# Performance work log

Hardware: AMD Instinct MI355X
Metric: run time of the kernel (lower is better)

Reference implementation:

```python
import jax, jax.numpy as jnp
import numpy as np

D = 1024      # input_dim == attention_dim == num_heads*head_dim
H = 16        # num_heads
HD = 64       # head_dim
FF = 4096     # ff_dim
EPS = 1e-5


def _layernorm(x, gamma, beta):
    mu = jnp.mean(x, axis=-1, keepdims=True)
    var = jnp.var(x, axis=-1, keepdims=True)
    return (x - mu) * jax.lax.rsqrt(var + EPS) * gamma + beta


def setup_inputs() -> dict:
    key = jax.random.key(0)
    ks = jax.random.split(key, 11)
    s_in = 1.0 / np.sqrt(D)
    s_ff = 1.0 / np.sqrt(FF)
    return {
        "x": jax.random.normal(ks[0], (2, 2048, D), dtype=jnp.float32),
        "w_qkv": jax.random.uniform(ks[1], (D, 3 * D), jnp.float32, -s_in, s_in),
        "b_qkv": jax.random.uniform(ks[2], (3 * D,), jnp.float32, -s_in, s_in),
        "w_o": jax.random.uniform(ks[3], (D, D), jnp.float32, -s_in, s_in),
        "b_o": jax.random.uniform(ks[4], (D,), jnp.float32, -s_in, s_in),
        "g1": jnp.ones((D,), jnp.float32),
        "be1": jnp.zeros((D,), jnp.float32),
        "w1": jax.random.uniform(ks[5], (D, FF), jnp.float32, -s_in, s_in),
        "b1": jax.random.uniform(ks[6], (FF,), jnp.float32, -s_in, s_in),
        "w2": jax.random.uniform(ks[7], (FF, D), jnp.float32, -s_ff, s_ff),
        "b2": jax.random.uniform(ks[8], (D,), jnp.float32, -s_ff, s_ff),
        "g2": jnp.ones((D,), jnp.float32),
        "be2": jnp.zeros((D,), jnp.float32),
    }


def reference(x, w_qkv, b_qkv, w_o, b_o, g1, be1, w1, b1, w2, b2, g2, be2):
    N, L, _ = x.shape
    qkv = x @ w_qkv + b_qkv                       # [N, L, 3D]
    q = qkv[..., :D].reshape(N, L, H, HD)
    k = qkv[..., D:2 * D].reshape(N, L, H, HD)
    v = qkv[..., 2 * D:].reshape(N, L, H, HD)
    scores = jnp.einsum('nqhd,nkhd->nhqk', q, k) / np.sqrt(HD)
    attn = jax.nn.softmax(scores, axis=-1)        # [N, H, L, L]
    out = jnp.einsum('nhql,nlhd->nqhd', attn, v).reshape(N, L, D)
    attn_out = out @ w_o + b_o
    # dropout is identity in eval mode
    h = _layernorm(attn_out + x, g1, be1)
    ff = jax.nn.relu(h @ w1 + b1) @ w2 + b2
    return _layernorm(h + ff, g2, be2)
```

## Files before the change

### kernel.cpp

```cpp
#include <hip/hip_runtime.h>
#include <cstddef>
#include <cstdint>

static constexpr int Dm   = 1024;
static constexpr int Hh   = 16;
static constexpr int HDd  = 64;
static constexpr int FFd  = 4096;
static constexpr int Ls   = 2048;
static constexpr int Nb   = 2;
static constexpr int Mrows = Nb * Ls;

typedef short bf16x8 __attribute__((ext_vector_type(8)));
typedef float f32x4  __attribute__((ext_vector_type(4)));

__device__ __forceinline__ ushort f2b(float f) {
    uint32_t u = __builtin_bit_cast(uint32_t, f);
    u = (u + 0x7FFFu + ((u >> 16) & 1u)) >> 16;
    return (ushort)u;
}
__device__ __forceinline__ ushort f2bf(float f) {
    return (ushort)((__builtin_bit_cast(uint32_t, f) + 0x8000u) >> 16);
}
__device__ __forceinline__ float b2f(ushort b) {
    return __builtin_bit_cast(float, (uint32_t)b << 16);
}

__device__ __forceinline__ void gl2lds16(const ushort* g, ushort* l) {
    __builtin_amdgcn_global_load_lds(
        (const __attribute__((address_space(1))) void*)g,
        (__attribute__((address_space(3))) void*)l, 16, 0, 0);
}

__global__ __launch_bounds__(256) void convert_bf16(
    const float* __restrict__ src, ushort* __restrict__ dst, int n)
{
    int i = (blockIdx.x * 256 + threadIdx.x) * 4;
    if (i >= n) return;
    float4 v = *(const float4*)(src + i);
    uint2 o;
    o.x = (uint32_t)f2b(v.x) | ((uint32_t)f2b(v.y) << 16);
    o.y = (uint32_t)f2b(v.z) | ((uint32_t)f2b(v.w) << 16);
    *(uint2*)(dst + i) = o;
}

__global__ __launch_bounds__(256) void transpose_bf16(
    const float* __restrict__ src, ushort* __restrict__ dst, int K, int N)
{
    __shared__ float t[32][33];
    const int k0 = blockIdx.y * 32, n0 = blockIdx.x * 32;
    const int tx = threadIdx.x & 31, ty = threadIdx.x >> 5;
    #pragma unroll
    for (int i = 0; i < 4; ++i)
        t[ty + i * 8][tx] = src[(size_t)(k0 + ty + i * 8) * N + n0 + tx];
    __syncthreads();
    #pragma unroll
    for (int i = 0; i < 4; ++i)
        dst[(size_t)(n0 + ty + i * 8) * K + k0 + tx] = f2b(t[tx][ty + i * 8]);
}

template <int TN, int RELU, int VOUT, int SPLITK>
__global__ __launch_bounds__(256) void gemm_mfma(
    const ushort* __restrict__ A, const ushort* __restrict__ Bt,
    const float* __restrict__ bias,
    ushort* __restrict__ Cb, ushort* __restrict__ vT, int M, int N, int K)
{
    constexpr int NT  = TN / 32;
    constexpr int BSZ = TN * 32;
    __shared__ __align__(16) ushort As[2 * 128 * 32];
    __shared__ __align__(16) ushort Bs[2 * BSZ];

    const int tid  = threadIdx.x;
    int bx, by;
    {
        const int gx = gridDim.x;
        const int nwg = gx * gridDim.y;
        const int lin = blockIdx.y * gx + blockIdx.x;
        const int swz = (lin & 7) * (nwg >> 3) + (lin >> 3);
        by = swz / gx; bx = swz - by * gx;
    }
    const int bm   = by * 128, bn = bx * TN;
    const int wave = tid >> 6, lane = tid & 63;
    const int wm = (wave & 1) * 64;
    const int wn = (wave >> 1) * (TN / 2);
    const int lr = lane & 15, lq = lane >> 4;

    const int KS   = K / SPLITK;
    const int Koff = (SPLITK > 1) ? blockIdx.z * KS : 0;

    const int rr = wave * 16 + (lane >> 2);
    const int sg = lane & 3;
    const ushort* Ag = A  + (size_t)(bm + rr) * K + Koff + sg * 8;
    const ushort* Bg = Bt + (size_t)(bn + rr) * K + Koff + sg * 8;

    f32x4 acc[4][NT];
    #pragma unroll
    for (int i = 0; i < 4; ++i)
        #pragma unroll
        for (int j = 0; j < NT; ++j)
            acc[i][j] = (f32x4){0.f, 0.f, 0.f, 0.f};

    gl2lds16(Ag,                  As + wave * 512);
    gl2lds16(Ag + (size_t)64 * K, As + 2048 + wave * 512);
    gl2lds16(Bg,                  Bs + wave * 512);
    if (TN == 128)
        gl2lds16(Bg + (size_t)64 * K, Bs + 2048 + wave * 512);

    int ib = 0;
    for (int k0 = 0; k0 < KS; k0 += 32, ib ^= 1) {
        __syncthreads();
        if (k0 + 32 < KS) {
            const int nb = ib ^ 1;
            gl2lds16(Ag + k0 + 32,                  As + nb * 4096 + wave * 512);
            gl2lds16(Ag + k0 + 32 + (size_t)64 * K, As + nb * 4096 + 2048 + wave * 512);
            gl2lds16(Bg + k0 + 32,                  Bs + nb * BSZ + wave * 512);
            if (TN == 128)
                gl2lds16(Bg + k0 + 32 + (size_t)64 * K, Bs + nb * BSZ + 2048 + wave * 512);
        }

        const ushort* Ar = As + ib * 4096;
        const ushort* Br = Bs + ib * BSZ;
        bf16x8 af[4], bf[NT];
        #pragma unroll
        for (int mt = 0; mt < 4; ++mt)
            af[mt] = *(const bf16x8*)(Ar + (wm + mt * 16 + lr) * 32 + lq * 8);
        #pragma unroll
        for (int nt = 0; nt < NT; ++nt)
            bf[nt] = *(const bf16x8*)(Br + (wn + nt * 16 + lr) * 32 + lq * 8);

        #pragma unroll
        for (int mt = 0; mt < 4; ++mt)
            #pragma unroll
            for (int nt = 0; nt < NT; ++nt)
                acc[mt][nt] = __builtin_amdgcn_mfma_f32_16x16x32_bf16(
                    af[mt], bf[nt], acc[mt][nt], 0, 0, 0);
    }

    if (SPLITK > 1) {
        ushort* Cp = Cb + (size_t)blockIdx.z * M * N;
        #pragma unroll
        for (int nt = 0; nt < NT; ++nt) {
            const int n = bn + wn + nt * 16 + lr;
            #pragma unroll
            for (int mt = 0; mt < 4; ++mt) {
                const int m0 = bm + wm + mt * 16 + lq * 4;
                #pragma unroll
                for (int r = 0; r < 4; ++r)
                    Cp[(size_t)(m0 + r) * N + n] = f2bf(acc[mt][nt][r]);
            }
        }
        return;
    }
    if (VOUT && bn >= 2 * Dm) {
        #pragma unroll
        for (int nt = 0; nt < NT; ++nt) {
            const int n = bn + wn + nt * 16 + lr;
            const float bv = bias[n];
            const int col = n - 2 * Dm;
            const int h = col >> 6, d = col & 63;
            #pragma unroll
            for (int mt = 0; mt < 4; ++mt) {
                const int m0 = bm + wm + mt * 16 + lq * 4;
                const int batch = m0 >> 11, key0 = m0 & (Ls - 1);
                ushort4 ob;
                ushort* op = (ushort*)&ob;
                #pragma unroll
                for (int r = 0; r < 4; ++r) op[r] = f2bf(acc[mt][nt][r] + bv);
                *(ushort4*)(vT + (((size_t)(batch * Hh + h)) * HDd + d) * Ls + key0) = ob;
            }
        }
        return;
    }
    #pragma unroll
    for (int nt = 0; nt < NT; ++nt) {
        const int n = bn + wn + nt * 16 + lr;
        const float bv = bias[n];
        #pragma unroll
        for (int mt = 0; mt < 4; ++mt) {
            const int m0 = bm + wm + mt * 16 + lq * 4;
            #pragma unroll
            for (int r = 0; r < 4; ++r) {
                float v = acc[mt][nt][r] + bv;
                if (RELU) v = fmaxf(v, 0.0f);
                Cb[(size_t)(m0 + r) * N + n] = f2bf(v);
            }
        }
    }
}

__global__ __launch_bounds__(256) void attn_mfma(
    const ushort* __restrict__ qkv, const ushort* __restrict__ vT,
    ushort* __restrict__ out)
{
    const int tid = threadIdx.x, wave = tid >> 6, lane = tid & 63;
    const int lr = lane & 15, lq = lane >> 4;
    int bx, h, n;
    {
        const int lin = (blockIdx.z * 16 + blockIdx.y) * 16 + blockIdx.x;
        const int swz = (lin & 7) * 64 + (lin >> 3);
        bx = swz & 15; h = (swz >> 4) & 15; n = swz >> 8;
    }
    const int q0 = bx * 128 + wave * 32;
    const size_t RS = 3 * Dm;
    const ushort* base  = qkv + (size_t)n * Ls * RS;
    const ushort* vbase = vT + (size_t)(n * Hh + h) * HDd * Ls;

    __shared__ __align__(16) ushort Kb[64 * 72];
    __shared__ __align__(16) ushort Vt[64 * 72];
    __shared__ __align__(16) ushort Pq[4][32 * 72];

    bf16x8 qf[2][2];
    {
        const float c = 0.18033688011112042f;
        #pragma unroll
        for (int qh = 0; qh < 2; ++qh) {
            const ushort* qg = base + (size_t)(q0 + qh * 16 + lr) * RS + h * HDd + lq * 8;
            bf16x8 t0 = *(const bf16x8*)(qg);
            bf16x8 t1 = *(const bf16x8*)(qg + 32);
            #pragma unroll
            for (int j = 0; j < 8; ++j) {
                qf[0][qh][j] = (short)f2b(b2f((ushort)t0[j]) * c);
                qf[1][qh][j] = (short)f2b(b2f((ushort)t1[j]) * c);
            }
        }
    }

    bf16x8 onesf;
    #pragma unroll
    for (int j = 0; j < 8; ++j) onesf[j] = (short)0x3F80;
    const f32x4 z4 = (f32x4){0.f, 0.f, 0.f, 0.f};

    f32x4 o[4][2];
    #pragma unroll
    for (int dt = 0; dt < 4; ++dt)
        #pragma unroll
        for (int qh = 0; qh < 2; ++qh)
            o[dt][qh] = (f32x4){0.f, 0.f, 0.f, 0.f};
    f32x4 dacc[2];
    dacc[0] = (f32x4){0.f, 0.f, 0.f, 0.f};
    dacc[1] = (f32x4){0.f, 0.f, 0.f, 0.f};

    const int srow = tid >> 2, ssg = tid & 3;
    const ushort* kg = base + (size_t)srow * RS + Dm + h * HDd;
    const ushort* vg = vbase + (size_t)srow * Ls;
    ushort* Pw = Pq[wave];

    int4 ka = *(const int4*)(kg + ssg * 8);
    int4 kb = *(const int4*)(kg + (ssg + 4) * 8);
    int4 va = *(const int4*)(vg + ssg * 8);
    int4 vb = *(const int4*)(vg + (ssg + 4) * 8);

    for (int kt = 0; kt < Ls; kt += 64) {
        __syncthreads();
        *(int4*)(Kb + srow * 72 + ssg * 8)       = ka;
        *(int4*)(Kb + srow * 72 + (ssg + 4) * 8) = kb;
        *(int4*)(Vt + srow * 72 + ssg * 8)       = va;
        *(int4*)(Vt + srow * 72 + (ssg + 4) * 8) = vb;
        __syncthreads();

        if (kt + 64 < Ls) {
            const ushort* kp = kg + (size_t)(kt + 64) * RS;
            const ushort* vp = vg + (kt + 64);
            ka = *(const int4*)(kp + ssg * 8);
            kb = *(const int4*)(kp + (ssg + 4) * 8);
            va = *(const int4*)(vp + ssg * 8);
            vb = *(const int4*)(vp + (ssg + 4) * 8);
        }

        f32x4 s[4][2];
        #pragma unroll
        for (int ks = 0; ks < 2; ++ks)
            #pragma unroll
            for (int mt = 0; mt < 4; ++mt) {
                bf16x8 kf = *(const bf16x8*)(Kb + (mt * 16 + lr) * 72 + ks * 32 + lq * 8);
                #pragma unroll
                for (int qh = 0; qh < 2; ++qh)
                    s[mt][qh] = __builtin_amdgcn_mfma_f32_16x16x32_bf16(
                        kf, qf[ks][qh], ks == 0 ? z4 : s[mt][qh], 0, 0, 0);
            }

        uint2 pb[4][2];
        #pragma unroll
        for (int mt = 0; mt < 4; ++mt)
            #pragma unroll
            for (int qh = 0; qh < 2; ++qh) {
                float p0 = exp2f(s[mt][qh][0]);
                float p1 = exp2f(s[mt][qh][1]);
                float p2 = exp2f(s[mt][qh][2]);
                float p3 = exp2f(s[mt][qh][3]);
                uint32_t w0, w1;
                asm("v_cvt_pk_bf16_f32 %0, %1, %2" : "=v"(w0) : "v"(p0), "v"(p1));
                asm("v_cvt_pk_bf16_f32 %0, %1, %2" : "=v"(w1) : "v"(p2), "v"(p3));
                pb[mt][qh].x = w0;
                pb[mt][qh].y = w1;
            }

        #pragma unroll
        for (int qh = 0; qh < 2; ++qh)
            #pragma unroll
            for (int mt = 0; mt < 4; ++mt)
                *(uint2*)(Pw + (qh * 16 + lr) * 72 + mt * 16 + lq * 4) = pb[mt][qh];

        #pragma unroll
        for (int ks = 0; ks < 2; ++ks) {
            bf16x8 pf[2];
            #pragma unroll
            for (int qh = 0; qh < 2; ++qh)
                pf[qh] = *(const bf16x8*)(Pw + (qh * 16 + lr) * 72 + ks * 32 + lq * 8);
            #pragma unroll
            for (int dt = 0; dt < 4; ++dt) {
                bf16x8 vf = *(const bf16x8*)(Vt + (dt * 16 + lr) * 72 + ks * 32 + lq * 8);
                #pragma unroll
                for (int qh = 0; qh < 2; ++qh)
                    o[dt][qh] = __builtin_amdgcn_mfma_f32_16x16x32_bf16(
                        vf, pf[qh], o[dt][qh], 0, 0, 0);
            }
            #pragma unroll
            for (int qh = 0; qh < 2; ++qh)
                dacc[qh] = __builtin_amdgcn_mfma_f32_16x16x32_bf16(
                    onesf, pf[qh], dacc[qh], 0, 0, 0);
        }
    }

    #pragma unroll
    for (int qh = 0; qh < 2; ++qh) {
        const float inv = 1.0f / dacc[qh][0];
        ushort* orow = out + (size_t)(n * Ls + q0 + qh * 16 + lr) * Dm + h * HDd;
        #pragma unroll
        for (int dt = 0; dt < 4; ++dt) {
            ushort4 ob;
            ushort* op = (ushort*)&ob;
            #pragma unroll
            for (int r = 0; r < 4; ++r) op[r] = f2bf(o[dt][qh][r] * inv);
            *(ushort4*)(orow + dt * 16 + lq * 4) = ob;
        }
    }
}

template <int OTHER_BF16, int OUT_F32>
__global__ __launch_bounds__(256) void add3_ln(
    const ushort* __restrict__ part, const void* __restrict__ other,
    const float* __restrict__ bias,
    const float* __restrict__ gamma, const float* __restrict__ beta,
    float* __restrict__ outf, ushort* __restrict__ outb)
{
    const int row = blockIdx.x;
    const int tid = threadIdx.x;

    ushort4 u0 = ((const ushort4*)(part + (size_t)row * Dm))[tid];
    ushort4 u1 = ((const ushort4*)(part + (size_t)Mrows * Dm + (size_t)row * Dm))[tid];
    float4  bv = ((const float4*)bias)[tid];

    float vo[4];
    if (OTHER_BF16) {
        ushort4 u = ((const ushort4*)((const ushort*)other + (size_t)row * Dm))[tid];
        vo[0] = b2f(u.x); vo[1] = b2f(u.y); vo[2] = b2f(u.z); vo[3] = b2f(u.w);
    } else {
        float4 f = ((const float4*)((const float*)other + (size_t)row * Dm))[tid];
        vo[0] = f.x; vo[1] = f.y; vo[2] = f.z; vo[3] = f.w;
    }
    float v[4];
    v[0] = b2f(u0.x) + b2f(u1.x) + bv.x + vo[0];
    v[1] = b2f(u0.y) + b2f(u1.y) + bv.y + vo[1];
    v[2] = b2f(u0.z) + b2f(u1.z) + bv.z + vo[2];
    v[3] = b2f(u0.w) + b2f(u1.w) + bv.w + vo[3];

    float s  = v[0] + v[1] + v[2] + v[3];
    float sq = v[0]*v[0] + v[1]*v[1] + v[2]*v[2] + v[3]*v[3];

    __shared__ float red[8];
    #pragma unroll
    for (int off = 32; off > 0; off >>= 1) {
        s  += __shfl_down(s, off);
        sq += __shfl_down(sq, off);
    }
    const int wv = tid >> 6;
    if ((tid & 63) == 0) { red[wv] = s; red[4 + wv] = sq; }
    __syncthreads();
    s  = red[0] + red[1] + red[2] + red[3];
    sq = red[4] + red[5] + red[6] + red[7];

    const float mu  = s * (1.0f / Dm);
    const float var = sq * (1.0f / Dm) - mu * mu;
    const float inv = rsqrtf(var + 1e-5f);

    const float4 g  = ((const float4*)gamma)[tid];
    const float4 be = ((const float4*)beta)[tid];
    float ov[4];
    ov[0] = (v[0] - mu) * inv * g.x + be.x;
    ov[1] = (v[1] - mu) * inv * g.y + be.y;
    ov[2] = (v[2] - mu) * inv * g.z + be.z;
    ov[3] = (v[3] - mu) * inv * g.w + be.w;
    if (OUT_F32) {
        float4 o4 = {ov[0], ov[1], ov[2], ov[3]};
        ((float4*)(outf + (size_t)row * Dm))[tid] = o4;
    } else {
        uint2 ob;
        ob.x = (uint32_t)f2bf(ov[0]) | ((uint32_t)f2bf(ov[1]) << 16);
        ob.y = (uint32_t)f2bf(ov[2]) | ((uint32_t)f2bf(ov[3]) << 16);
        *(uint2*)(outb + (size_t)row * Dm + tid * 4) = ob;
    }
}

extern "C" void kernel_launch(void* const* d_in, const int* in_sizes, int n_in,
                              void* d_out, int out_size, void* d_ws, size_t ws_size,
                              hipStream_t stream)
{
    const float* x     = (const float*)d_in[0];
    const float* w_qkv = (const float*)d_in[1];
    const float* b_qkv = (const float*)d_in[2];
    const float* w_o   = (const float*)d_in[3];
    const float* b_o   = (const float*)d_in[4];
    const float* g1    = (const float*)d_in[5];
    const float* be1   = (const float*)d_in[6];
    const float* w1    = (const float*)d_in[7];
    const float* b1    = (const float*)d_in[8];
    const float* w2    = (const float*)d_in[9];
    const float* b2    = (const float*)d_in[10];
    const float* g2    = (const float*)d_in[11];
    const float* be2   = (const float*)d_in[12];
    float* out = (float*)d_out;

    char* p = (char*)d_ws;
    ushort* qkvb  = (ushort*)p;  p += (size_t)Mrows * 3 * Dm * 2;
    ushort* attnb = (ushort*)p;  p += (size_t)Mrows * Dm * 2;
    ushort* part  = (ushort*)p;  p += (size_t)2 * Mrows * Dm * 2;
    ushort* hb    = (ushort*)p;  p += (size_t)Mrows * Dm * 2;
    ushort* ffb   = (ushort*)p;  p += (size_t)Mrows * FFd * 2;
    ushort* xb    = (ushort*)p;  p += (size_t)Mrows * Dm * 2;
    ushort* wqkvT = (ushort*)p;  p += (size_t)(3 * Dm) * Dm * 2;
    ushort* woT   = (ushort*)p;  p += (size_t)Dm * Dm * 2;
    ushort* w1T   = (ushort*)p;  p += (size_t)FFd * Dm * 2;
    ushort* w2T   = (ushort*)p;  p += (size_t)Dm * FFd * 2;
    ushort* vTg   = (ushort*)p;  p += (size_t)Mrows * Dm * 2;

    convert_bf16<<<dim3(Mrows * Dm / 1024), dim3(256), 0, stream>>>(x, xb, Mrows * Dm);
    transpose_bf16<<<dim3(3 * Dm / 32, Dm / 32), dim3(256), 0, stream>>>(w_qkv, wqkvT, Dm, 3 * Dm);
    transpose_bf16<<<dim3(Dm / 32, Dm / 32),     dim3(256), 0, stream>>>(w_o, woT, Dm, Dm);
    transpose_bf16<<<dim3(FFd / 32, Dm / 32),    dim3(256), 0, stream>>>(w1, w1T, Dm, FFd);
    transpose_bf16<<<dim3(Dm / 32, FFd / 32),    dim3(256), 0, stream>>>(w2, w2T, FFd, Dm);

    gemm_mfma<128, 0, 1, 1><<<dim3(3 * Dm / 128, Mrows / 128), dim3(256), 0, stream>>>(
        xb, wqkvT, b_qkv, qkvb, vTg, Mrows, 3 * Dm, Dm);

    attn_mfma<<<dim3(Ls / 128, Hh, Nb), dim3(256), 0, stream>>>(qkvb, vTg, attnb);

    gemm_mfma<64, 0, 0, 2><<<dim3(Dm / 64, Mrows / 128, 2), dim3(256), 0, stream>>>(
        attnb, woT, nullptr, part, nullptr, Mrows, Dm, Dm);

    add3_ln<0, 0><<<dim3(Mrows), dim3(256), 0, stream>>>(
        part, x, b_o, g1, be1, nullptr, hb);

    gemm_mfma<128, 1, 0, 1><<<dim3(FFd / 128, Mrows / 128), dim3(256), 0, stream>>>(
        hb, w1T, b1, ffb, nullptr, Mrows, FFd, Dm);

    gemm_mfma<64, 0, 0, 2><<<dim3(Dm / 64, Mrows / 128, 2), dim3(256), 0, stream>>>(
        ffb, w2T, nullptr, part, nullptr, Mrows, Dm, FFd);

    add3_ln<1, 1><<<dim3(Mrows), dim3(256), 0, stream>>>(
        part, hb, b2, g2, be2, out, nullptr);
}
```

Before: 386.0 us.

## Split attention over two KV halves and add a combine kernel

The attention kernel now splits the key/value sequence into two halves, doubling the grid from 512 to 1024 blocks so more workgroups fill the GPU. Each half writes unnormalized fp32 partial outputs and softmax denominators into reused workspace buffers, and a new combine kernel sums them, normalizes, and writes bf16. This is valid because the kernel uses no running max; it exponentiates raw pre-scaled scores. The exp2 call is also switched to the hardware builtin when available. The cost is an extra launch and a roughly 32MB fp32 partial buffer that must be written and read back.

```diff
diff --git a/kernel.cpp b/kernel.cpp
--- a/kernel.cpp
+++ b/kernel.cpp
@@ -12,6 +12,12 @@
 
 typedef short bf16x8 __attribute__((ext_vector_type(8)));
 typedef float f32x4  __attribute__((ext_vector_type(4)));
+
+#if __has_builtin(__builtin_amdgcn_exp2f)
+#define EXP2(x) __builtin_amdgcn_exp2f(x)
+#else
+#define EXP2(x) exp2f(x)
+#endif
 
 __device__ __forceinline__ ushort f2b(float f) {
     uint32_t u = __builtin_bit_cast(uint32_t, f);
@@ -189,16 +195,18 @@
 
 __global__ __launch_bounds__(256) void attn_mfma(
     const ushort* __restrict__ qkv, const ushort* __restrict__ vT,
-    ushort* __restrict__ out)
+    float* __restrict__ npart, float* __restrict__ dpart)
 {
     const int tid = threadIdx.x, wave = tid >> 6, lane = tid & 63;
     const int lr = lane & 15, lq = lane >> 4;
-    int bx, h, n;
+    int bx, h, z;
     {
         const int lin = (blockIdx.z * 16 + blockIdx.y) * 16 + blockIdx.x;
-        const int swz = (lin & 7) * 64 + (lin >> 3);
-        bx = swz & 15; h = (swz >> 4) & 15; n = swz >> 8;
-    }
+        const int swz = (lin & 7) * 128 + (lin >> 3);
+        bx = swz & 15; h = (swz >> 4) & 15; z = swz >> 8;
+    }
+    const int n = z >> 1, kv = z & 1;
+    const int kt0 = kv * (Ls / 2);
     const int q0 = bx * 128 + wave * 32;
     const size_t RS = 3 * Dm;
     const ushort* base  = qkv + (size_t)n * Ls * RS;
@@ -244,12 +252,16 @@
     const ushort* vg = vbase + (size_t)srow * Ls;
     ushort* Pw = Pq[wave];
 
-    int4 ka = *(const int4*)(kg + ssg * 8);
-    int4 kb = *(const int4*)(kg + (ssg + 4) * 8);
-    int4 va = *(const int4*)(vg + ssg * 8);
-    int4 vb = *(const int4*)(vg + (ssg + 4) * 8);
-
-    for (int kt = 0; kt < Ls; kt += 64) {
+    {
+        const ushort* kp = kg + (size_t)kt0 * RS;
+        const ushort* vp = vg + kt0;
+    }
+    int4 ka = *(const int4*)(kg + (size_t)kt0 * RS + ssg * 8);
+    int4 kb = *(const int4*)(kg + (size_t)kt0 * RS + (ssg + 4) * 8);
+    int4 va = *(const int4*)(vg + kt0 + ssg * 8);
+    int4 vb = *(const int4*)(vg + kt0 + (ssg + 4) * 8);
+
+    for (int kt = kt0; kt < kt0 + Ls / 2; kt += 64) {
         __syncthreads();
         *(int4*)(Kb + srow * 72 + ssg * 8)       = ka;
         *(int4*)(Kb + srow * 72 + (ssg + 4) * 8) = kb;
@@ -257,7 +269,7 @@
         *(int4*)(Vt + srow * 72 + (ssg + 4) * 8) = vb;
         __syncthreads();
 
-        if (kt + 64 < Ls) {
+        if (kt + 64 < kt0 + Ls / 2) {
             const ushort* kp = kg + (size_t)(kt + 64) * RS;
             const ushort* vp = vg + (kt + 64);
             ka = *(const int4*)(kp + ssg * 8);
@@ -283,10 +295,10 @@
         for (int mt = 0; mt < 4; ++mt)
             #pragma unroll
             for (int qh = 0; qh < 2; ++qh) {
-                float p0 = exp2f(s[mt][qh][0]);
-                float p1 = exp2f(s[mt][qh][1]);
-                float p2 = exp2f(s[mt][qh][2]);
-                float p3 = exp2f(s[mt][qh][3]);
+                float p0 = EXP2(s[mt][qh][0]);
+                float p1 = EXP2(s[mt][qh][1]);
+                float p2 = EXP2(s[mt][qh][2]);
+                float p3 = EXP2(s[mt][qh][3]);
                 uint32_t w0, w1;
                 asm("v_cvt_pk_bf16_f32 %0, %1, %2" : "=v"(w0) : "v"(p0), "v"(p1));
                 asm("v_cvt_pk_bf16_f32 %0, %1, %2" : "=v"(w1) : "v"(p2), "v"(p3));
@@ -321,19 +333,43 @@
         }
     }
 
+    const int idx = kv * Nb + n;
     #pragma unroll
     for (int qh = 0; qh < 2; ++qh) {
-        const float inv = 1.0f / dacc[qh][0];
-        ushort* orow = out + (size_t)(n * Ls + q0 + qh * 16 + lr) * Dm + h * HDd;
+        float* nrow = npart + ((size_t)idx * Ls + q0 + qh * 16 + lr) * Dm + h * HDd;
         #pragma unroll
         for (int dt = 0; dt < 4; ++dt) {
-            ushort4 ob;
-            ushort* op = (ushort*)&ob;
-            #pragma unroll
-            for (int r = 0; r < 4; ++r) op[r] = f2bf(o[dt][qh][r] * inv);
-            *(ushort4*)(orow + dt * 16 + lq * 4) = ob;
-        }
-    }
+            float4 o4 = {o[dt][qh][0], o[dt][qh][1], o[dt][qh][2], o[dt][qh][3]};
+            *(float4*)(nrow + dt * 16 + lq * 4) = o4;
+        }
+        if (lane < 16)
+            dpart[((size_t)idx * Hh + h) * Ls + q0 + qh * 16 + lane] = dacc[qh][0];
+    }
+}
+
+__global__ __launch_bounds__(256) void attn_combine(
+    const float* __restrict__ npart, const float* __restrict__ dpart,
+    ushort* __restrict__ out)
+{
+    const int row = blockIdx.x;
+    const int tid = threadIdx.x;
+    const int n = row >> 11, q = row & (Ls - 1);
+    const int h = tid >> 4;
+
+    const size_t b0 = ((size_t)(0 * Nb + n) * Ls + q) * Dm;
+    const size_t b1 = ((size_t)(1 * Nb + n) * Ls + q) * Dm;
+    float4 a = ((const float4*)(npart + b0))[tid];
+    float4 b = ((const float4*)(npart + b1))[tid];
+    const float d0 = dpart[((size_t)(0 * Nb + n) * Hh + h) * Ls + q];
+    const float d1 = dpart[((size_t)(1 * Nb + n) * Hh + h) * Ls + q];
+    const float inv = 1.0f / (d0 + d1);
+
+    ushort4 ob;
+    ob.x = f2bf((a.x + b.x) * inv);
+    ob.y = f2bf((a.y + b.y) * inv);
+    ob.z = f2bf((a.z + b.z) * inv);
+    ob.w = f2bf((a.w + b.w) * inv);
+    *(ushort4*)(out + (size_t)row * Dm + tid * 4) = ob;
 }
 
 template <int OTHER_BF16, int OUT_F32>
@@ -433,6 +469,9 @@
     ushort* w2T   = (ushort*)p;  p += (size_t)Dm * FFd * 2;
     ushort* vTg   = (ushort*)p;  p += (size_t)Mrows * Dm * 2;
 
+    float* npart = (float*)ffb;
+    float* dpart = (float*)part;
+
     convert_bf16<<<dim3(Mrows * Dm / 1024), dim3(256), 0, stream>>>(x, xb, Mrows * Dm);
     transpose_bf16<<<dim3(3 * Dm / 32, Dm / 32), dim3(256), 0, stream>>>(w_qkv, wqkvT, Dm, 3 * Dm);
     transpose_bf16<<<dim3(Dm / 32, Dm / 32),     dim3(256), 0, stream>>>(w_o, woT, Dm, Dm);
@@ -442,7 +481,8 @@
     gemm_mfma<128, 0, 1, 1><<<dim3(3 * Dm / 128, Mrows / 128), dim3(256), 0, stream>>>(
         xb, wqkvT, b_qkv, qkvb, vTg, Mrows, 3 * Dm, Dm);
 
-    attn_mfma<<<dim3(Ls / 128, Hh, Nb), dim3(256), 0, stream>>>(qkvb, vTg, attnb);
+    attn_mfma<<<dim3(Ls / 128, Hh, 2 * Nb), dim3(256), 0, stream>>>(qkvb, vTg, npart, dpart);
+    attn_combine<<<dim3(Mrows), dim3(256), 0, stream>>>(npart, dpart, attnb);
 
     gemm_mfma<64, 0, 0, 2><<<dim3(Dm / 64, Mrows / 128, 2), dim3(256), 0, stream>>>(
         attnb, woT, nullptr, part, nullptr, Mrows, Dm, Dm);
```

New measurement: 386.3 us. Within noise of the previous version (+0.1%).
